# Kernel optimization log

Hardware: AMD Instinct MI355X
Metric: run time of the kernel (lower is better)

## Reference

```python
import jax, jax.numpy as jnp
import numpy as np

N_ITERS = 3
EPS_ATTN = 1e-8
LN_EPS = 1e-5  # torch LayerNorm default

def _ln(x, w, b):
    mu = jnp.mean(x, axis=-1, keepdims=True)
    var = jnp.mean(jnp.square(x - mu), axis=-1, keepdims=True)
    return (x - mu) * jax.lax.rsqrt(var + LN_EPS) * w + b

def setup_inputs() -> dict:
    key = jax.random.key(0)
    ks = jax.random.split(key, 10)
    B, N, F, D, K = 64, 4096, 256, 128, 8
    return {
        "inputs": jax.random.normal(ks[0], (B, N, F), jnp.float32),
        "slot_init": jax.random.normal(ks[1], (1, K, D), jnp.float32) * 0.02,
        "Wq": jax.random.normal(ks[2], (D, D), jnp.float32) * (1.0 / np.sqrt(D)),
        "Wk": jax.random.normal(ks[3], (F, D), jnp.float32) * (1.0 / np.sqrt(F)),
        "Wv": jax.random.normal(ks[4], (F, D), jnp.float32) * (1.0 / np.sqrt(F)),
        "gru_wi": jax.random.normal(ks[5], (D, 3 * D), jnp.float32) * (1.0 / np.sqrt(D)),
        "gru_wh": jax.random.normal(ks[6], (D, 3 * D), jnp.float32) * (1.0 / np.sqrt(D)),
        "gru_bi": jnp.zeros((3 * D,), jnp.float32),
        "gru_bh": jnp.zeros((3 * D,), jnp.float32),
        "ln_in_w": jnp.ones((F,), jnp.float32),
        "ln_in_b": jnp.zeros((F,), jnp.float32),
        "ln_slots_w": jnp.ones((D,), jnp.float32),
        "ln_slots_b": jnp.zeros((D,), jnp.float32),
        "ln_mlp_w": jnp.ones((D,), jnp.float32),
        "ln_mlp_b": jnp.zeros((D,), jnp.float32),
        "mlp_w1": jax.random.normal(ks[7], (D, 2 * D), jnp.float32) * (1.0 / np.sqrt(D)),
        "mlp_b1": jnp.zeros((2 * D,), jnp.float32),
        "mlp_w2": jax.random.normal(ks[8], (2 * D, D), jnp.float32) * (1.0 / np.sqrt(2 * D)),
        "mlp_b2": jnp.zeros((D,), jnp.float32),
    }

def reference(inputs, slot_init, Wq, Wk, Wv, gru_wi, gru_wh, gru_bi, gru_bh,
              ln_in_w, ln_in_b, ln_slots_w, ln_slots_b, ln_mlp_w, ln_mlp_b,
              mlp_w1, mlp_b1, mlp_w2, mlp_b2):
    B, N, _ = inputs.shape
    D = Wq.shape[0]
    scale = jnp.asarray(D ** 0.5, inputs.dtype)
    x = _ln(inputs, ln_in_w, ln_in_b)
    k = x @ Wk            # [B, N, D]
    v = x @ Wv            # [B, N, D]
    slots = jnp.broadcast_to(slot_init, (B,) + slot_init.shape[1:])
    for _ in range(N_ITERS):
        slots_prev = slots
        q = _ln(slots, ln_slots_w, ln_slots_b) @ Wq         # [B, K, D]
        logits = jnp.einsum('bnd,bkd->bnk', k, q) / scale   # [B, N, K]
        attn = jax.nn.softmax(logits, axis=-1) + EPS_ATTN   # softmax over slots
        attn = attn / jnp.sum(attn, axis=1, keepdims=True)  # normalize over inputs
        updates = jnp.einsum('bnk,bnd->bkd', attn, v)       # [B, K, D]
        # GRUCell: x=updates, h=slots_prev (torch gate order: r, z, n)
        gx = updates @ gru_wi + gru_bi                      # [B, K, 3D]
        gh = slots_prev @ gru_wh + gru_bh
        r = jax.nn.sigmoid(gx[..., :D] + gh[..., :D])
        z = jax.nn.sigmoid(gx[..., D:2 * D] + gh[..., D:2 * D])
        n = jnp.tanh(gx[..., 2 * D:] + r * gh[..., 2 * D:])
        slots = (1.0 - z) * n + z * slots_prev
        h = jax.nn.relu(_ln(slots, ln_mlp_w, ln_mlp_b) @ mlp_w1 + mlp_b1)
        slots = slots + h @ mlp_w2 + mlp_b2
    return slots
```

## Files before the change

### kernel.cpp

```cpp
#include <hip/hip_runtime.h>
#include <math.h>

#define NB 64
#define NN 4096
#define NF 256
#define ND 128
#define NK 8
#define NCHUNK 16
#define CHROWS 256
#define MT 64

typedef unsigned int uint;
typedef unsigned short ushort;
typedef __attribute__((ext_vector_type(8))) short short8;
typedef __attribute__((ext_vector_type(4))) float floatx4;

constexpr float LN_EPS_C   = 1e-5f;
constexpr float EPS_ATTN_C = 1e-8f;
constexpr float INV_SCALE  = 0.08838834764831845f;

__device__ __forceinline__ float sigmoidf_(float x) { return 1.f / (1.f + expf(-x)); }
__device__ __forceinline__ ushort f2bf(float x) {
    uint u = __float_as_uint(x);
    return (ushort)((u + 0x7FFFu + ((u >> 16) & 1u)) >> 16);
}
__device__ __forceinline__ float bflo(uint u) { return __uint_as_float(u << 16); }
__device__ __forceinline__ float bfhi(uint u) { return __uint_as_float(u & 0xFFFF0000u); }

__global__ void init_slots_k(const float* __restrict__ init, float* __restrict__ slots) {
    int i = blockIdx.x * 256 + threadIdx.x;
    slots[i] = init[i & (NK * ND - 1)];
}

__global__ void wconv_k(const float* __restrict__ Wk, const float* __restrict__ Wv,
                        ushort* __restrict__ wt2) {
    int idx = blockIdx.x * 64 + threadIdx.x;
    int c16 = idx >> 9, ks = (idx >> 6) & 7, lane = idx & 63;
    int c = c16 * 16 + (lane & 15);
    int f0 = ks * 32 + (lane >> 4) * 8;
    ushort tmp[8];
#pragma unroll
    for (int j = 0; j < 8; ++j) {
        int f = f0 + j;
        float v = (c < ND) ? Wk[(size_t)f * ND + c] : Wv[(size_t)f * ND + (c - ND)];
        tmp[j] = f2bf(v);
    }
    *(uint4*)(wt2 + (size_t)idx * 8) = *(uint4*)tmp;
}

__global__ __launch_bounds__(256) void ln_project_mfma(
    const float* __restrict__ inp, const ushort* __restrict__ wt2,
    const float* __restrict__ lw, const float* __restrict__ lb,
    uint* __restrict__ kt2, ushort* __restrict__ vout) {
    __shared__ ushort As[MT][264];
    int t = threadIdx.x;
    size_t rowbase = (size_t)blockIdx.x * MT;
    size_t bidx = rowbase >> 12;
    size_t nbase = rowbase & (NN - 1);

    {
        int rloc = t >> 4, seg = t & 15;
        const float4* lw4 = (const float4*)lw;
        const float4* lb4 = (const float4*)lb;
#pragma unroll
        for (int p = 0; p < 4; ++p) {
            int r = p * 16 + rloc;
            const float4* rowp = (const float4*)(inp + (rowbase + r) * NF);
            float4 xv[4];
            float sum = 0.f, sq = 0.f;
#pragma unroll
            for (int i = 0; i < 4; ++i) {
                xv[i] = rowp[seg * 4 + i];
                sum += xv[i].x + xv[i].y + xv[i].z + xv[i].w;
                sq += xv[i].x * xv[i].x + xv[i].y * xv[i].y + xv[i].z * xv[i].z + xv[i].w * xv[i].w;
            }
#pragma unroll
            for (int m = 8; m >= 1; m >>= 1) {
                sum += __shfl_xor(sum, m, 64);
                sq  += __shfl_xor(sq,  m, 64);
            }
            float mu = sum * (1.f / NF);
            float var = sq * (1.f / NF) - mu * mu;
            float rs = rsqrtf(var + LN_EPS_C);
#pragma unroll
            for (int i = 0; i < 4; ++i) {
                float4 w = lw4[seg * 4 + i], bb = lb4[seg * 4 + i], x = xv[i];
                float o0 = (x.x - mu) * rs * w.x + bb.x;
                float o1 = (x.y - mu) * rs * w.y + bb.y;
                float o2 = (x.z - mu) * rs * w.z + bb.z;
                float o3 = (x.w - mu) * rs * w.w + bb.w;
                uint2 pk;
                pk.x = (uint)f2bf(o0) | ((uint)f2bf(o1) << 16);
                pk.y = (uint)f2bf(o2) | ((uint)f2bf(o3) << 16);
                *(uint2*)&As[r][seg * 16 + i * 4] = pk;
            }
        }
    }
    __syncthreads();

    int w = t >> 6, lane = t & 63;
    int frow = lane & 15, q = lane >> 4;
    floatx4 acc[4][4];
#pragma unroll
    for (int mt = 0; mt < 4; ++mt)
#pragma unroll
        for (int nt = 0; nt < 4; ++nt) acc[mt][nt] = (floatx4)0.f;

#pragma unroll
    for (int ks = 0; ks < 8; ++ks) {
        short8 a[4], b[4];
#pragma unroll
        for (int nt = 0; nt < 4; ++nt)
            b[nt] = *(const short8*)(wt2 + ((((size_t)(w * 4 + nt) * 8 + ks) * 64 + lane) * 8));
#pragma unroll
        for (int mt = 0; mt < 4; ++mt)
            a[mt] = *(const short8*)&As[mt * 16 + frow][ks * 32 + q * 8];
#pragma unroll
        for (int mt = 0; mt < 4; ++mt)
#pragma unroll
            for (int nt = 0; nt < 4; ++nt)
                acc[mt][nt] = __builtin_amdgcn_mfma_f32_16x16x32_bf16(a[mt], b[nt], acc[mt][nt], 0, 0, 0);
    }

    __syncthreads();

    if (w < 2) {
        int cbase = w * 64;
#pragma unroll
        for (int mt = 0; mt < 4; ++mt)
#pragma unroll
            for (int nt = 0; nt < 4; ++nt) {
                int c = cbase + nt * 16 + frow;
                uint u01 = (uint)f2bf(acc[mt][nt][0]) | ((uint)f2bf(acc[mt][nt][1]) << 16);
                uint u23 = (uint)f2bf(acc[mt][nt][2]) | ((uint)f2bf(acc[mt][nt][3]) << 16);
                uint p01 = __shfl_xor(u01, 1, 64);
                uint p23 = __shfl_xor(u23, 1, 64);
                if ((frow & 1) == 0) {
                    uint4 out;
                    out.x = (u01 & 0xFFFFu) | (p01 << 16);
                    out.y = (u01 >> 16) | (p01 & 0xFFFF0000u);
                    out.z = (u23 & 0xFFFFu) | (p23 << 16);
                    out.w = (u23 >> 16) | (p23 & 0xFFFF0000u);
                    size_t nloc = nbase + mt * 16 + q * 4;
                    *(uint4*)(kt2 + (bidx * 64 + (size_t)(c >> 1)) * NN + nloc) = out;
                }
            }
    } else {
        int cbase = (w & 1) * 64;
#pragma unroll
        for (int mt = 0; mt < 4; ++mt)
#pragma unroll
            for (int nt = 0; nt < 4; ++nt) {
                int c = cbase + nt * 16 + frow;
#pragma unroll
                for (int i = 0; i < 4; ++i)
                    As[mt * 16 + q * 4 + i][c] = f2bf(acc[mt][nt][i]);
            }
    }
    __syncthreads();

    {
        int r = t >> 2, part = t & 3;
#pragma unroll
        for (int u = 0; u < 4; ++u) {
            uint4 val = *(const uint4*)&As[r][part * 32 + u * 8];
            *(uint4*)(vout + (rowbase + r) * ND + part * 32 + u * 8) = val;
        }
    }
}

__global__ __launch_bounds__(64) void q_kernel(
    const float* __restrict__ slots, const float* __restrict__ Wq,
    const float* __restrict__ lw, const float* __restrict__ lb,
    float* __restrict__ qout) {
    __shared__ float sln[ND];
    int bk = blockIdx.x;
    int t = threadIdx.x;
    const float* sp = slots + (size_t)bk * ND;
    float s0 = sp[t], s1 = sp[t + 64];
    float sum = s0 + s1, sq = s0 * s0 + s1 * s1;
#pragma unroll
    for (int m = 1; m < 64; m <<= 1) {
        sum += __shfl_xor(sum, m, 64);
        sq  += __shfl_xor(sq,  m, 64);
    }
    float mu = sum * (1.f / ND);
    float var = sq * (1.f / ND) - mu * mu;
    float rs = rsqrtf(var + LN_EPS_C);
    sln[t]      = (s0 - mu) * rs * lw[t]      + lb[t];
    sln[t + 64] = (s1 - mu) * rs * lw[t + 64] + lb[t + 64];
    __syncthreads();
    float q0 = 0.f, q1 = 0.f;
    for (int dd = 0; dd < ND; ++dd) {
        float v = sln[dd];
        q0 += v * Wq[dd * ND + t];
        q1 += v * Wq[dd * ND + 64 + t];
    }
    qout[(size_t)bk * ND + t] = q0;
    qout[(size_t)bk * ND + 64 + t] = q1;
}

__global__ __launch_bounds__(256) void attn_kernel(
    const uint* __restrict__ kt2, const ushort* __restrict__ vbuf,
    const float* __restrict__ qbuf, float* __restrict__ pU,
    float* __restrict__ pS) {
    __shared__ __align__(16) float attn_s[CHROWS * NK];
    __shared__ __align__(16) float qs2[64 * 16];
    __shared__ __align__(16) float red_s[4][16][64];
    __shared__ float sS[4][NK];
    int t = threadIdx.x;
    int chunk = blockIdx.x, b = blockIdx.y;
    int n = chunk * CHROWS + t;
    int w = t >> 6, lane = t & 63;

#pragma unroll
    for (int p = 0; p < 4; ++p) {
        int idx = p * 256 + t;
        int kk = idx >> 7, d = idx & 127;
        qs2[(d >> 1) * 16 + kk * 2 + (d & 1)] = qbuf[(size_t)b * NK * ND + idx];
    }
    __syncthreads();

    {
        const uint* ktp = kt2 + (size_t)b * 64 * NN + n;
        float lg[NK];
#pragma unroll
        for (int kk = 0; kk < NK; ++kk) lg[kk] = 0.f;
#pragma unroll 8
        for (int j = 0; j < 64; ++j) {
            uint kr = ktp[(size_t)j * NN];
            float k0 = bflo(kr), k1 = bfhi(kr);
            const float4* qp = (const float4*)(qs2 + j * 16);
#pragma unroll
            for (int c = 0; c < 4; ++c) {
                float4 qq = qp[c];
                lg[2 * c]     += k0 * qq.x + k1 * qq.y;
                lg[2 * c + 1] += k0 * qq.z + k1 * qq.w;
            }
        }
        float mx = -1e30f;
#pragma unroll
        for (int kk = 0; kk < NK; ++kk) { lg[kk] *= INV_SCALE; mx = fmaxf(mx, lg[kk]); }
        float se = 0.f;
        float e[NK];
#pragma unroll
        for (int kk = 0; kk < NK; ++kk) { e[kk] = expf(lg[kk] - mx); se += e[kk]; }
        float inv = 1.f / se;
#pragma unroll
        for (int kk = 0; kk < NK; ++kk) e[kk] = e[kk] * inv + EPS_ATTN_C;
        ((float4*)attn_s)[t * 2]     = make_float4(e[0], e[1], e[2], e[3]);
        ((float4*)attn_s)[t * 2 + 1] = make_float4(e[4], e[5], e[6], e[7]);

#pragma unroll
        for (int m = 1; m < 64; m <<= 1) {
#pragma unroll
            for (int kk = 0; kk < NK; ++kk) e[kk] += __shfl_xor(e[kk], m, 64);
        }
        if (lane == 0) {
#pragma unroll
            for (int kk = 0; kk < NK; ++kk) sS[w][kk] = e[kk];
        }
    }
    __syncthreads();

    {
        float ua[16];
#pragma unroll
        for (int a = 0; a < 16; ++a) ua[a] = 0.f;
        const uint* vp = (const uint*)(vbuf + ((size_t)b * NN + (size_t)chunk * CHROWS + w * 64) * ND) + lane;
        const float4* ap = (const float4*)(attn_s + (w * 64) * NK);
        for (int nn2 = 0; nn2 < 64; ++nn2) {
            uint vr = vp[(size_t)nn2 * (ND / 2)];
            float v0 = bflo(vr), v1 = bfhi(vr);
            float4 aA = ap[nn2 * 2];
            float4 aB = ap[nn2 * 2 + 1];
            ua[0]  += aA.x * v0; ua[1]  += aA.x * v1;
            ua[2]  += aA.y * v0; ua[3]  += aA.y * v1;
            ua[4]  += aA.z * v0; ua[5]  += aA.z * v1;
            ua[6]  += aA.w * v0; ua[7]  += aA.w * v1;
            ua[8]  += aB.x * v0; ua[9]  += aB.x * v1;
            ua[10] += aB.y * v0; ua[11] += aB.y * v1;
            ua[12] += aB.z * v0; ua[13] += aB.z * v1;
            ua[14] += aB.w * v0; ua[15] += aB.w * v1;
        }
#pragma unroll
        for (int a = 0; a < 16; ++a) red_s[w][a][lane] = ua[a];
    }
    __syncthreads();

    {
        size_t pb = ((size_t)chunk * NB + b) * (NK * ND);
#pragma unroll
        for (int i = 0; i < 4; ++i) {
            int slot = i * 256 + t;
            int a = slot >> 6, l = slot & 63;
            float s = red_s[0][a][l] + red_s[1][a][l] + red_s[2][a][l] + red_s[3][a][l];
            int kk = a >> 1, r = a & 1;
            pU[pb + (size_t)kk * ND + 2 * l + r] = s;
        }
        if (t < NK) pS[((size_t)chunk * NB + b) * NK + t] = sS[0][t] + sS[1][t] + sS[2][t] + sS[3][t];
    }
}

__global__ __launch_bounds__(256) void finish_kernel(
    const float* __restrict__ pU, const float* __restrict__ pS,
    const float* __restrict__ slots_in, const float* __restrict__ wi,
    const float* __restrict__ wh, const float* __restrict__ bi,
    const float* __restrict__ bh, const float* __restrict__ lnw,
    const float* __restrict__ lnb, const float* __restrict__ w1,
    const float* __restrict__ b1, const float* __restrict__ w2,
    const float* __restrict__ b2, float* __restrict__ slots_out,
    const float* __restrict__ Wq, const float* __restrict__ lqw,
    const float* __restrict__ lqb, float* __restrict__ qout, int compute_q) {
    __shared__ float updL[ND], spL[ND], lnL[ND], hL[2 * ND], lnQ[ND];
    __shared__ float part[6][2][ND];
    __shared__ float Up[2][ND], odp[2][ND], qp_[2][ND];
    __shared__ float red[2], red2[2];
    int bk = blockIdx.x;
    int b = bk >> 3, kk = bk & 7;
    int t = threadIdx.x;
    int d = t & 127, half = t >> 7;

    float U = 0.f;
#pragma unroll
    for (int c = half * 8; c < half * 8 + 8; ++c)
        U += pU[((size_t)c * NB + b) * (NK * ND) + kk * ND + d];
    Up[half][d] = U;
    float S = 0.f;
#pragma unroll
    for (int c = 0; c < NCHUNK; ++c) S += pS[((size_t)c * NB + b) * NK + kk];
    float spd = slots_in[(size_t)bk * ND + d];
    if (half == 0) spL[d] = spd;
    __syncthreads();
    float upd = (Up[0][d] + Up[1][d]) / S;
    if (half == 0) updL[d] = upd;
    __syncthreads();

    float a0 = 0.f, a1 = 0.f, a2 = 0.f, a3 = 0.f, a4 = 0.f, a5 = 0.f;
    {
        int dd0 = half * 64;
        for (int dd = dd0; dd < dd0 + 64; ++dd) {
            float u = updL[dd], s = spL[dd];
            const float* wip = wi + (size_t)dd * 3 * ND;
            const float* whp = wh + (size_t)dd * 3 * ND;
            a0 += u * wip[d];          a3 += s * whp[d];
            a1 += u * wip[ND + d];     a4 += s * whp[ND + d];
            a2 += u * wip[2 * ND + d]; a5 += s * whp[2 * ND + d];
        }
    }
    part[0][half][d] = a0; part[1][half][d] = a1; part[2][half][d] = a2;
    part[3][half][d] = a3; part[4][half][d] = a4; part[5][half][d] = a5;
    __syncthreads();
    float gxr = bi[d]          + part[0][0][d] + part[0][1][d];
    float gxz = bi[ND + d]     + part[1][0][d] + part[1][1][d];
    float gxn = bi[2 * ND + d] + part[2][0][d] + part[2][1][d];
    float ghr = bh[d]          + part[3][0][d] + part[3][1][d];
    float ghz = bh[ND + d]     + part[4][0][d] + part[4][1][d];
    float ghn = bh[2 * ND + d] + part[5][0][d] + part[5][1][d];
    float r_ = sigmoidf_(gxr + ghr);
    float z_ = sigmoidf_(gxz + ghz);
    float nn_ = tanhf(gxn + r_ * ghn);
    float snew = (1.f - z_) * nn_ + z_ * spd;

    if (half == 0) {
        int wid = d >> 6;
        float sum = snew, sq = snew * snew;
#pragma unroll
        for (int m = 1; m < 64; m <<= 1) {
            sum += __shfl_xor(sum, m, 64);
            sq  += __shfl_xor(sq,  m, 64);
        }
        if ((d & 63) == 0) { red[wid] = sum; red2[wid] = sq; }
    }
    __syncthreads();
    {
        float tot = red[0] + red[1], totq = red2[0] + red2[1];
        float mu = tot * (1.f / ND);
        float var = totq * (1.f / ND) - mu * mu;
        float rs = rsqrtf(var + LN_EPS_C);
        if (half == 0) lnL[d] = (snew - mu) * rs * lnw[d] + lnb[d];
    }
    __syncthreads();

    {
        float h0 = b1[t];
        for (int dd = 0; dd < ND; ++dd) h0 += lnL[dd] * w1[(size_t)dd * 2 * ND + t];
        hL[t] = fmaxf(h0, 0.f);
    }
    __syncthreads();

    {
        float od_p = 0.f;
        int j0 = half * ND;
        for (int j = j0; j < j0 + ND; ++j) od_p += hL[j] * w2[(size_t)j * ND + d];
        odp[half][d] = od_p;
    }
    __syncthreads();
    float od = snew + b2[d] + odp[0][d] + odp[1][d];
    if (half == 0) slots_out[(size_t)bk * ND + d] = od;

    if (compute_q) {
        if (half == 0) {
            int wid = d >> 6;
            float s2 = od, q2 = od * od;
#pragma unroll
            for (int m = 1; m < 64; m <<= 1) {
                s2 += __shfl_xor(s2, m, 64);
                q2 += __shfl_xor(q2, m, 64);
            }
            if ((d & 63) == 0) { red[wid] = s2; red2[wid] = q2; }
        }
        __syncthreads();
        {
            float tq = red[0] + red[1], tqq = red2[0] + red2[1];
            float muq = tq * (1.f / ND);
            float vq = tqq * (1.f / ND) - muq * muq;
            float rsq = rsqrtf(vq + LN_EPS_C);
            if (half == 0) lnQ[d] = (od - muq) * rsq * lqw[d] + lqb[d];
        }
        __syncthreads();
        {
            float qc = 0.f;
            int dq0 = half * 64;
            for (int dd = dq0; dd < dq0 + 64; ++dd) qc += lnQ[dd] * Wq[(size_t)dd * ND + d];
            qp_[half][d] = qc;
        }
        __syncthreads();
        if (half == 0) qout[(size_t)bk * ND + d] = qp_[0][d] + qp_[1][d];
    }
}

extern "C" void kernel_launch(void* const* d_in, const int* in_sizes, int n_in,
                              void* d_out, int out_size, void* d_ws, size_t ws_size,
                              hipStream_t stream) {
    const float* inp       = (const float*)d_in[0];
    const float* slot_init = (const float*)d_in[1];
    const float* Wq        = (const float*)d_in[2];
    const float* Wk        = (const float*)d_in[3];
    const float* Wv        = (const float*)d_in[4];
    const float* gru_wi    = (const float*)d_in[5];
    const float* gru_wh    = (const float*)d_in[6];
    const float* gru_bi    = (const float*)d_in[7];
    const float* gru_bh    = (const float*)d_in[8];
    const float* ln_in_w   = (const float*)d_in[9];
    const float* ln_in_b   = (const float*)d_in[10];
    const float* ln_sl_w   = (const float*)d_in[11];
    const float* ln_sl_b   = (const float*)d_in[12];
    const float* ln_ml_w   = (const float*)d_in[13];
    const float* ln_ml_b   = (const float*)d_in[14];
    const float* mlp_w1    = (const float*)d_in[15];
    const float* mlp_b1    = (const float*)d_in[16];
    const float* mlp_w2    = (const float*)d_in[17];
    const float* mlp_b2    = (const float*)d_in[18];

    char* wsb = (char*)d_ws;
    uint* kt2   = (uint*)wsb;
    ushort* vb  = (ushort*)(wsb + (size_t)NB * 64 * NN * 4);
    ushort* wt2 = vb + (size_t)NB * NN * ND;
    float* qb   = (float*)(wt2 + (size_t)NF * NF);
    float* sl   = qb + (size_t)NB * NK * ND;
    float* pU   = sl + (size_t)NB * NK * ND;
    float* pS   = pU + (size_t)NCHUNK * NB * NK * ND;

    init_slots_k<<<(NB * NK * ND) / 256, 256, 0, stream>>>(slot_init, sl);
    wconv_k<<<128, 64, 0, stream>>>(Wk, Wv, wt2);
    ln_project_mfma<<<(NB * NN) / MT, 256, 0, stream>>>(inp, wt2, ln_in_w, ln_in_b, kt2, vb);
    q_kernel<<<NB * NK, 64, 0, stream>>>(sl, Wq, ln_sl_w, ln_sl_b, qb);

    for (int it = 0; it < 3; ++it) {
        attn_kernel<<<dim3(NCHUNK, NB), 256, 0, stream>>>(kt2, vb, qb, pU, pS);
        float* outp = (it == 2) ? (float*)d_out : sl;
        finish_kernel<<<NB * NK, 256, 0, stream>>>(pU, pS, sl, gru_wi, gru_wh,
                                                   gru_bi, gru_bh, ln_ml_w, ln_ml_b,
                                                   mlp_w1, mlp_b1, mlp_w2, mlp_b2, outp,
                                                   Wq, ln_sl_w, ln_sl_b, qb, (it < 2) ? 1 : 0);
    }
}
```

Before: 718.7 us.

## Stage K tiles through LDS with register prefetch; widen finish kernel to 512 threads

In the attention kernel, the per-thread strided 4-byte loads of K are replaced by cooperative 16-byte vector loads. These are staged through a padded LDS tile in four 16-row rounds, and the next round is prefetched into registers while the current one is consumed. The reduction buffer now reuses the K staging LDS, and the V accumulation loop is unrolled by 4. The finish kernel goes from 256 to 512 threads, splitting its GRU, MLP and Q matvecs four ways (two ways for the first MLP layer) to add parallelism on a latency-bound tail. The cost is extra barriers and LDS traffic per round in attention, and more cross-partition reduction work in finish.

```diff
diff --git a/kernel.cpp b/kernel.cpp
--- a/kernel.cpp
+++ b/kernel.cpp
@@ -204,33 +204,50 @@
     const uint* __restrict__ kt2, const ushort* __restrict__ vbuf,
     const float* __restrict__ qbuf, float* __restrict__ pU,
     float* __restrict__ pS) {
+    __shared__ __align__(16) uint kst[16 * 260];
     __shared__ __align__(16) float attn_s[CHROWS * NK];
     __shared__ __align__(16) float qs2[64 * 16];
-    __shared__ __align__(16) float red_s[4][16][64];
     __shared__ float sS[4][NK];
+    float* red_s = (float*)kst;
+
     int t = threadIdx.x;
     int chunk = blockIdx.x, b = blockIdx.y;
-    int n = chunk * CHROWS + t;
     int w = t >> 6, lane = t & 63;
-
-#pragma unroll
-    for (int p = 0; p < 4; ++p) {
-        int idx = p * 256 + t;
-        int kk = idx >> 7, d = idx & 127;
-        qs2[(d >> 1) * 16 + kk * 2 + (d & 1)] = qbuf[(size_t)b * NK * ND + idx];
-    }
-    __syncthreads();
-
-    {
-        const uint* ktp = kt2 + (size_t)b * 64 * NN + n;
-        float lg[NK];
-#pragma unroll
-        for (int kk = 0; kk < NK; ++kk) lg[kk] = 0.f;
-#pragma unroll 8
-        for (int j = 0; j < 64; ++j) {
-            uint kr = ktp[(size_t)j * NN];
+    int p = t >> 4, sub = t & 15;
+
+    const uint* kbase = kt2 + (size_t)b * 64 * NN + (size_t)chunk * CHROWS + sub * 4;
+    uint4 pf[4];
+#pragma unroll
+    for (int i = 0; i < 4; ++i)
+        pf[i] = *(const uint4*)(kbase + (size_t)p * NN + i * 64);
+
+#pragma unroll
+    for (int pp = 0; pp < 4; ++pp) {
+        int idx = pp * 256 + t;
+        int kq = idx >> 7, dq = idx & 127;
+        qs2[(dq >> 1) * 16 + kq * 2 + (dq & 1)] = qbuf[(size_t)b * NK * ND + idx];
+    }
+
+    float lg[NK];
+#pragma unroll
+    for (int kk = 0; kk < NK; ++kk) lg[kk] = 0.f;
+
+    for (int r = 0; r < 4; ++r) {
+        __syncthreads();
+#pragma unroll
+        for (int i = 0; i < 4; ++i)
+            *(uint4*)(kst + p * 260 + sub * 4 + i * 64) = pf[i];
+        __syncthreads();
+        if (r < 3) {
+#pragma unroll
+            for (int i = 0; i < 4; ++i)
+                pf[i] = *(const uint4*)(kbase + (size_t)((r + 1) * 16 + p) * NN + i * 64);
+        }
+#pragma unroll
+        for (int j = 0; j < 16; ++j) {
+            uint kr = kst[j * 260 + t];
             float k0 = bflo(kr), k1 = bfhi(kr);
-            const float4* qp = (const float4*)(qs2 + j * 16);
+            const float4* qp = (const float4*)(qs2 + (r * 16 + j) * 16);
 #pragma unroll
             for (int c = 0; c < 4; ++c) {
                 float4 qq = qp[c];
@@ -238,6 +255,9 @@
                 lg[2 * c + 1] += k0 * qq.z + k1 * qq.w;
             }
         }
+    }
+
+    {
         float mx = -1e30f;
 #pragma unroll
         for (int kk = 0; kk < NK; ++kk) { lg[kk] *= INV_SCALE; mx = fmaxf(mx, lg[kk]); }
@@ -250,7 +270,6 @@
         for (int kk = 0; kk < NK; ++kk) e[kk] = e[kk] * inv + EPS_ATTN_C;
         ((float4*)attn_s)[t * 2]     = make_float4(e[0], e[1], e[2], e[3]);
         ((float4*)attn_s)[t * 2 + 1] = make_float4(e[4], e[5], e[6], e[7]);
-
 #pragma unroll
         for (int m = 1; m < 64; m <<= 1) {
 #pragma unroll
@@ -269,6 +288,7 @@
         for (int a = 0; a < 16; ++a) ua[a] = 0.f;
         const uint* vp = (const uint*)(vbuf + ((size_t)b * NN + (size_t)chunk * CHROWS + w * 64) * ND) + lane;
         const float4* ap = (const float4*)(attn_s + (w * 64) * NK);
+#pragma unroll 4
         for (int nn2 = 0; nn2 < 64; ++nn2) {
             uint vr = vp[(size_t)nn2 * (ND / 2)];
             float v0 = bflo(vr), v1 = bfhi(vr);
@@ -284,7 +304,7 @@
             ua[14] += aB.w * v0; ua[15] += aB.w * v1;
         }
 #pragma unroll
-        for (int a = 0; a < 16; ++a) red_s[w][a][lane] = ua[a];
+        for (int a = 0; a < 16; ++a) red_s[(w * 16 + a) * 64 + lane] = ua[a];
     }
     __syncthreads();
 
@@ -294,7 +314,8 @@
         for (int i = 0; i < 4; ++i) {
             int slot = i * 256 + t;
             int a = slot >> 6, l = slot & 63;
-            float s = red_s[0][a][l] + red_s[1][a][l] + red_s[2][a][l] + red_s[3][a][l];
+            float s = red_s[(0 * 16 + a) * 64 + l] + red_s[(1 * 16 + a) * 64 + l] +
+                      red_s[(2 * 16 + a) * 64 + l] + red_s[(3 * 16 + a) * 64 + l];
             int kk = a >> 1, r = a & 1;
             pU[pb + (size_t)kk * ND + 2 * l + r] = s;
         }
@@ -302,7 +323,7 @@
     }
 }
 
-__global__ __launch_bounds__(256) void finish_kernel(
+__global__ __launch_bounds__(512) void finish_kernel(
     const float* __restrict__ pU, const float* __restrict__ pS,
     const float* __restrict__ slots_in, const float* __restrict__ wi,
     const float* __restrict__ wh, const float* __restrict__ bi,
@@ -312,34 +333,36 @@
     const float* __restrict__ b2, float* __restrict__ slots_out,
     const float* __restrict__ Wq, const float* __restrict__ lqw,
     const float* __restrict__ lqb, float* __restrict__ qout, int compute_q) {
-    __shared__ float updL[ND], spL[ND], lnL[ND], hL[2 * ND], lnQ[ND];
-    __shared__ float part[6][2][ND];
-    __shared__ float Up[2][ND], odp[2][ND], qp_[2][ND];
+    __shared__ float updL[ND], spL[ND], lnL[ND], lnQ[ND], hL[2 * ND];
+    __shared__ float Up[4][ND];
+    __shared__ float part[4][6][ND];
+    __shared__ float hpart[2][2 * ND];
+    __shared__ float odp[4][ND], qp_[4][ND];
     __shared__ float red[2], red2[2];
     int bk = blockIdx.x;
     int b = bk >> 3, kk = bk & 7;
     int t = threadIdx.x;
-    int d = t & 127, half = t >> 7;
+    int d = t & 127, qd = t >> 7;
 
     float U = 0.f;
 #pragma unroll
-    for (int c = half * 8; c < half * 8 + 8; ++c)
+    for (int c = qd * 4; c < qd * 4 + 4; ++c)
         U += pU[((size_t)c * NB + b) * (NK * ND) + kk * ND + d];
-    Up[half][d] = U;
+    Up[qd][d] = U;
     float S = 0.f;
 #pragma unroll
     for (int c = 0; c < NCHUNK; ++c) S += pS[((size_t)c * NB + b) * NK + kk];
     float spd = slots_in[(size_t)bk * ND + d];
-    if (half == 0) spL[d] = spd;
-    __syncthreads();
-    float upd = (Up[0][d] + Up[1][d]) / S;
-    if (half == 0) updL[d] = upd;
+    if (t < ND) spL[d] = spd;
+    __syncthreads();
+    float upd = (Up[0][d] + Up[1][d] + Up[2][d] + Up[3][d]) / S;
+    if (t < ND) updL[d] = upd;
     __syncthreads();
 
     float a0 = 0.f, a1 = 0.f, a2 = 0.f, a3 = 0.f, a4 = 0.f, a5 = 0.f;
     {
-        int dd0 = half * 64;
-        for (int dd = dd0; dd < dd0 + 64; ++dd) {
+        int dd0 = qd * 32;
+        for (int dd = dd0; dd < dd0 + 32; ++dd) {
             float u = updL[dd], s = spL[dd];
             const float* wip = wi + (size_t)dd * 3 * ND;
             const float* whp = wh + (size_t)dd * 3 * ND;
@@ -348,21 +371,21 @@
             a2 += u * wip[2 * ND + d]; a5 += s * whp[2 * ND + d];
         }
     }
-    part[0][half][d] = a0; part[1][half][d] = a1; part[2][half][d] = a2;
-    part[3][half][d] = a3; part[4][half][d] = a4; part[5][half][d] = a5;
-    __syncthreads();
-    float gxr = bi[d]          + part[0][0][d] + part[0][1][d];
-    float gxz = bi[ND + d]     + part[1][0][d] + part[1][1][d];
-    float gxn = bi[2 * ND + d] + part[2][0][d] + part[2][1][d];
-    float ghr = bh[d]          + part[3][0][d] + part[3][1][d];
-    float ghz = bh[ND + d]     + part[4][0][d] + part[4][1][d];
-    float ghn = bh[2 * ND + d] + part[5][0][d] + part[5][1][d];
+    part[qd][0][d] = a0; part[qd][1][d] = a1; part[qd][2][d] = a2;
+    part[qd][3][d] = a3; part[qd][4][d] = a4; part[qd][5][d] = a5;
+    __syncthreads();
+    float gxr = bi[d]          + part[0][0][d] + part[1][0][d] + part[2][0][d] + part[3][0][d];
+    float gxz = bi[ND + d]     + part[0][1][d] + part[1][1][d] + part[2][1][d] + part[3][1][d];
+    float gxn = bi[2 * ND + d] + part[0][2][d] + part[1][2][d] + part[2][2][d] + part[3][2][d];
+    float ghr = bh[d]          + part[0][3][d] + part[1][3][d] + part[2][3][d] + part[3][3][d];
+    float ghz = bh[ND + d]     + part[0][4][d] + part[1][4][d] + part[2][4][d] + part[3][4][d];
+    float ghn = bh[2 * ND + d] + part[0][5][d] + part[1][5][d] + part[2][5][d] + part[3][5][d];
     float r_ = sigmoidf_(gxr + ghr);
     float z_ = sigmoidf_(gxz + ghz);
     float nn_ = tanhf(gxn + r_ * ghn);
     float snew = (1.f - z_) * nn_ + z_ * spd;
 
-    if (half == 0) {
+    if (t < ND) {
         int wid = d >> 6;
         float sum = snew, sq = snew * snew;
 #pragma unroll
@@ -378,29 +401,33 @@
         float mu = tot * (1.f / ND);
         float var = totq * (1.f / ND) - mu * mu;
         float rs = rsqrtf(var + LN_EPS_C);
-        if (half == 0) lnL[d] = (snew - mu) * rs * lnw[d] + lnb[d];
-    }
-    __syncthreads();
-
-    {
-        float h0 = b1[t];
-        for (int dd = 0; dd < ND; ++dd) h0 += lnL[dd] * w1[(size_t)dd * 2 * ND + t];
-        hL[t] = fmaxf(h0, 0.f);
-    }
+        if (t < ND) lnL[d] = (snew - mu) * rs * lnw[d] + lnb[d];
+    }
+    __syncthreads();
+
+    {
+        int o = t & 255, h = t >> 8;
+        float h0 = 0.f;
+        for (int dd = h * 64; dd < h * 64 + 64; ++dd)
+            h0 += lnL[dd] * w1[(size_t)dd * 2 * ND + o];
+        hpart[h][o] = h0;
+    }
+    __syncthreads();
+    if (t < 2 * ND) hL[t] = fmaxf(b1[t] + hpart[0][t] + hpart[1][t], 0.f);
     __syncthreads();
 
     {
         float od_p = 0.f;
-        int j0 = half * ND;
-        for (int j = j0; j < j0 + ND; ++j) od_p += hL[j] * w2[(size_t)j * ND + d];
-        odp[half][d] = od_p;
-    }
-    __syncthreads();
-    float od = snew + b2[d] + odp[0][d] + odp[1][d];
-    if (half == 0) slots_out[(size_t)bk * ND + d] = od;
+        int j0 = qd * 64;
+        for (int j = j0; j < j0 + 64; ++j) od_p += hL[j] * w2[(size_t)j * ND + d];
+        odp[qd][d] = od_p;
+    }
+    __syncthreads();
+    float od = snew + b2[d] + odp[0][d] + odp[1][d] + odp[2][d] + odp[3][d];
+    if (t < ND) slots_out[(size_t)bk * ND + d] = od;
 
     if (compute_q) {
-        if (half == 0) {
+        if (t < ND) {
             int wid = d >> 6;
             float s2 = od, q2 = od * od;
 #pragma unroll
@@ -416,17 +443,17 @@
             float muq = tq * (1.f / ND);
             float vq = tqq * (1.f / ND) - muq * muq;
             float rsq = rsqrtf(vq + LN_EPS_C);
-            if (half == 0) lnQ[d] = (od - muq) * rsq * lqw[d] + lqb[d];
+            if (t < ND) lnQ[d] = (od - muq) * rsq * lqw[d] + lqb[d];
         }
         __syncthreads();
         {
             float qc = 0.f;
-            int dq0 = half * 64;
-            for (int dd = dq0; dd < dq0 + 64; ++dd) qc += lnQ[dd] * Wq[(size_t)dd * ND + d];
-            qp_[half][d] = qc;
+            int dq0 = qd * 32;
+            for (int dd = dq0; dd < dq0 + 32; ++dd) qc += lnQ[dd] * Wq[(size_t)dd * ND + d];
+            qp_[qd][d] = qc;
         }
         __syncthreads();
-        if (half == 0) qout[(size_t)bk * ND + d] = qp_[0][d] + qp_[1][d];
+        if (t < ND) qout[(size_t)bk * ND + d] = qp_[0][d] + qp_[1][d] + qp_[2][d] + qp_[3][d];
     }
 }
 
@@ -470,7 +497,7 @@
     for (int it = 0; it < 3; ++it) {
         attn_kernel<<<dim3(NCHUNK, NB), 256, 0, stream>>>(kt2, vb, qb, pU, pS);
         float* outp = (it == 2) ? (float*)d_out : sl;
-        finish_kernel<<<NB * NK, 256, 0, stream>>>(pU, pS, sl, gru_wi, gru_wh,
+        finish_kernel<<<NB * NK, 512, 0, stream>>>(pU, pS, sl, gru_wi, gru_wh,
                                                    gru_bi, gru_bh, ln_ml_w, ln_ml_b,
                                                    mlp_w1, mlp_b1, mlp_w2, mlp_b2, outp,
                                                    Wq, ln_sl_w, ln_sl_b, qb, (it < 2) ? 1 : 0);
```

Measured after the change: 688.8 us. -4.2%, faster.
